# Performance work log

Hardware: AMD Instinct MI355X
Metric: run time of the kernel (lower is better)

Reference implementation:

```python
import jax, jax.numpy as jnp
import numpy as np

B, S, D, H = 4, 2048, 1024, 16
HD = D // H

def rotate_half(x):
    x1, x2 = jnp.split(x, 2, axis=-1)
    return jnp.concatenate((-x2, x1), axis=-1)

def apply_rope(x, cos, sin):
    # x: [B,H,S,hd]; cos/sin: [S,hd] -> broadcast over B,H
    return x * cos[None, None] + rotate_half(x) * sin[None, None]

def setup_inputs() -> dict:
    key = jax.random.key(0)
    ks = jax.random.split(key, 8)
    x = jax.random.normal(ks[0], (B, S, D), dtype=jnp.float32)
    mask = jnp.triu(jnp.ones((S, S), dtype=bool), k=1)  # True = masked (causal)
    pos = jnp.arange(S, dtype=jnp.float32)[:, None]
    inv = 1.0 / (10000.0 ** (jnp.arange(0, HD, 2, dtype=jnp.float32) / HD))
    ang = pos * inv[None, :]  # [S, hd/2]
    ang = jnp.concatenate([ang, ang], axis=-1)  # [S, hd]
    rope_cos = jnp.cos(ang)
    rope_sin = jnp.sin(ang)
    scale = 1.0 / np.sqrt(D)
    Wq = jax.random.normal(ks[1], (D, D), dtype=jnp.float32) * scale
    Wk = jax.random.normal(ks[2], (D, D), dtype=jnp.float32) * scale
    Wv = jax.random.normal(ks[3], (D, D), dtype=jnp.float32) * scale
    Wo = jax.random.normal(ks[4], (D, D), dtype=jnp.float32) * scale
    z = jnp.zeros((D,), dtype=jnp.float32)
    return {"x": x, "mask": mask, "rope_cos": rope_cos, "rope_sin": rope_sin,
            "Wq": Wq, "bq": z, "Wk": Wk, "bk": z, "Wv": Wv, "bv": z, "Wo": Wo, "bo": z}

def reference(x, mask, rope_cos, rope_sin, Wq, bq, Wk, bk, Wv, bv, Wo, bo):
    b, s, d = x.shape
    def proj(W, bias):
        y = x @ W.T + bias  # torch Linear: x W^T + b
        return y.reshape(b, s, H, HD).transpose(0, 2, 1, 3)  # [B,H,S,hd]
    Q = apply_rope(proj(Wq, bq), rope_cos, rope_sin)
    K = apply_rope(proj(Wk, bk), rope_cos, rope_sin)
    V = proj(Wv, bv)
    scores = jnp.einsum('bhqd,bhkd->bhqk', Q, K) / jnp.sqrt(jnp.float32(HD))
    scores = jnp.where(mask[None, None], -jnp.inf, scores)
    attn = jax.nn.softmax(scores, axis=-1)
    ctx = jnp.einsum('bhqk,bhkd->bhqd', attn, V)
    ctx = ctx.transpose(0, 2, 1, 3).reshape(b, s, d)
    return ctx @ Wo.T + bo
```

## Files before the change

kernel.cpp:

```cpp
#include <hip/hip_runtime.h>
#include <hip/hip_bf16.h>

#define S_LEN 2048
#define D_MODEL 1024
#define NH 16
#define HDIM 64
#define B_SZ 4

typedef __attribute__((ext_vector_type(8))) short bf16x8;
typedef __attribute__((ext_vector_type(4))) float f32x4;

__device__ inline void gld16(const __hip_bfloat16* g, __hip_bfloat16* l) {
    __builtin_amdgcn_global_load_lds(
        (const __attribute__((address_space(1))) unsigned int*)g,
        (__attribute__((address_space(3))) unsigned int*)l, 16, 0, 0);
}

__device__ inline unsigned int pkbf(float a, float b) {
    float2 f; f.x = a; f.y = b;
    __hip_bfloat162 h = __float22bfloat162_rn(f);
    union { __hip_bfloat162 h; unsigned int u; } cv; cv.h = h; return cv.u;
}

__global__ __launch_bounds__(256) void f2bf4_kernel(const float4* __restrict__ in,
                                                    __hip_bfloat162* __restrict__ out,
                                                    int n4) {
    int i = blockIdx.x * 256 + threadIdx.x;
    if (i < n4) {
        float4 v = in[i];
        __hip_bfloat162 a, b;
        a.x = __float2bfloat16(v.x); a.y = __float2bfloat16(v.y);
        b.x = __float2bfloat16(v.z); b.y = __float2bfloat16(v.w);
        out[2 * i]     = a;
        out[2 * i + 1] = b;
    }
}

__global__ __launch_bounds__(256) void f2bfw_kernel(
    const float4* __restrict__ w0, const float4* __restrict__ w1,
    const float4* __restrict__ w2, const float4* __restrict__ w3,
    __hip_bfloat162* __restrict__ o0, __hip_bfloat162* __restrict__ o1,
    __hip_bfloat162* __restrict__ o2, __hip_bfloat162* __restrict__ o3) {
    const int z = blockIdx.y;
    const float4* in = (z == 0) ? w0 : (z == 1) ? w1 : (z == 2) ? w2 : w3;
    __hip_bfloat162* out = (z == 0) ? o0 : (z == 1) ? o1 : (z == 2) ? o2 : o3;
    int i = blockIdx.x * 256 + threadIdx.x;
    float4 v = in[i];
    __hip_bfloat162 a, b;
    a.x = __float2bfloat16(v.x); a.y = __float2bfloat16(v.y);
    b.x = __float2bfloat16(v.z); b.y = __float2bfloat16(v.w);
    out[2 * i]     = a;
    out[2 * i + 1] = b;
}

__device__ inline void gemm_mainloop(const __hip_bfloat16* __restrict__ X,
                                     const __hip_bfloat16* __restrict__ W,
                                     __hip_bfloat16* As, __hip_bfloat16* Bs,
                                     int m0, int n0, f32x4 acc[4][4]) {
    const int tid = threadIdx.x;
    const int wv = tid >> 6, lane = tid & 63, l15 = lane & 15, quad = lane >> 4;
    const int rw = (wv >> 1) * 64, cw = (wv & 1) * 64;
    for (int k0 = 0; k0 < D_MODEL; k0 += 32) {
        __syncthreads();
#pragma unroll
        for (int i = 0; i < 2; i++) {
            int l = tid + 256 * i;
            int row = l >> 2, c8 = (l & 3) * 8;
            gld16(&X[(size_t)(m0 + row) * D_MODEL + k0 + c8], &As[row * 32 + c8]);
            gld16(&W[(size_t)(n0 + row) * D_MODEL + k0 + c8], &Bs[row * 32 + c8]);
        }
        __syncthreads();
        bf16x8 af[4], bfr[4];
#pragma unroll
        for (int t = 0; t < 4; t++)
            af[t] = *(const bf16x8*)&As[(rw + t * 16 + l15) * 32 + quad * 8];
#pragma unroll
        for (int t = 0; t < 4; t++)
            bfr[t] = *(const bf16x8*)&Bs[(cw + t * 16 + l15) * 32 + quad * 8];
#pragma unroll
        for (int mt = 0; mt < 4; mt++)
#pragma unroll
            for (int nt = 0; nt < 4; nt++)
                acc[mt][nt] = __builtin_amdgcn_mfma_f32_16x16x32_bf16(
                    af[mt], bfr[nt], acc[mt][nt], 0, 0, 0);
    }
}

#define PT 136
__global__ __launch_bounds__(256) void qkv_kernel(
    const __hip_bfloat16* __restrict__ X,
    const __hip_bfloat16* __restrict__ W0, const __hip_bfloat16* __restrict__ W1,
    const __hip_bfloat16* __restrict__ W2,
    const float* __restrict__ b0, const float* __restrict__ b1,
    const float* __restrict__ b2,
    const float* __restrict__ rc, const float* __restrict__ rs,
    __hip_bfloat16* __restrict__ Qo, __hip_bfloat16* __restrict__ Ko,
    __hip_bfloat16* __restrict__ Vo) {
    __shared__ __hip_bfloat16 pool[64 * PT];
    __hip_bfloat16* As = pool;
    __hip_bfloat16* Bs = pool + 4096;
    const int z = blockIdx.z;
    const __hip_bfloat16* W = (z == 0) ? W0 : ((z == 1) ? W1 : W2);
    const float* bias = (z == 0) ? b0 : ((z == 1) ? b1 : b2);
    f32x4 acc[4][4];
#pragma unroll
    for (int i = 0; i < 4; i++)
#pragma unroll
        for (int j = 0; j < 4; j++) acc[i][j] = (f32x4){0.f, 0.f, 0.f, 0.f};
    const int m0 = blockIdx.x * 128, n0 = blockIdx.y * 128;
    gemm_mainloop(X, W, As, Bs, m0, n0, acc);

    const int tid = threadIdx.x;
    const int wv = tid >> 6, lane = tid & 63, l15 = lane & 15, quad = lane >> 4;
    const int rw = (wv >> 1) * 64, cw = (wv & 1) * 64;

    if (z == 2) {
        __hip_bfloat16* T = pool;
        const int b = m0 >> 11, s0l = m0 & (S_LEN - 1);
#pragma unroll
        for (int hn = 0; hn < 2; hn++) {
            __syncthreads();
            if ((wv & 1) == hn) {
#pragma unroll
                for (int mt = 0; mt < 4; mt++)
#pragma unroll
                    for (int nt = 0; nt < 4; nt++)
#pragma unroll
                        for (int r = 0; r < 4; r++) {
                            int dl = nt * 16 + l15;
                            int ml = rw + mt * 16 + quad * 4 + r;
                            T[dl * PT + ml] =
                                __float2bfloat16(acc[mt][nt][r] + bias[n0 + hn * 64 + dl]);
                        }
            }
            __syncthreads();
            const int d = tid >> 2, sc = tid & 3;
            const int h = (n0 >> 6) + hn;
            size_t gb = ((size_t)((b * NH + h) * HDIM + d)) * S_LEN + s0l + sc * 32;
#pragma unroll
            for (int j = 0; j < 4; j++) {
                bf16x8 v = *(const bf16x8*)&T[d * PT + sc * 32 + j * 8];
                *(bf16x8*)&Vo[gb + j * 8] = v;
            }
        }
    } else {
        __hip_bfloat16* dst = (z == 0) ? Qo : Ko;
        const float qs = (z == 0) ? 0.18033688011112042f : 1.0f;
#pragma unroll
        for (int mt = 0; mt < 4; mt++)
#pragma unroll
            for (int r = 0; r < 4; r++) {
                int m = m0 + rw + mt * 16 + quad * 4 + r;
                int s = m & (S_LEN - 1), b = m >> 11;
#pragma unroll
                for (int nt = 0; nt < 2; nt++) {
                    int n1 = n0 + cw + nt * 16 + l15;
                    int h = n1 >> 6, hd1 = n1 & 63;
                    float y1 = acc[mt][nt][r] + bias[n1];
                    float y2 = acc[mt][nt + 2][r] + bias[n1 + 32];
                    float c1 = rc[s * HDIM + hd1], s1 = rs[s * HDIM + hd1];
                    float c2 = rc[s * HDIM + hd1 + 32], s2 = rs[s * HDIM + hd1 + 32];
                    size_t base = (((size_t)(b * NH + h)) * S_LEN + s) * HDIM;
                    dst[base + hd1]      = __float2bfloat16((y1 * c1 - y2 * s1) * qs);
                    dst[base + hd1 + 32] = __float2bfloat16((y2 * c2 + y1 * s2) * qs);
                }
            }
    }
}

#define SWZ(r, c) (((r) << 6) + ((c) ^ (((r) & 7) << 3)))
__global__ __launch_bounds__(256) void attn_kernel(
    const __hip_bfloat16* __restrict__ Q, const __hip_bfloat16* __restrict__ K,
    const __hip_bfloat16* __restrict__ VT, __hip_bfloat16* __restrict__ CTX) {
    __shared__ __hip_bfloat16 Kl[2][64 * 64];
    __shared__ __hip_bfloat16 Vl[2][64 * 64];
    __shared__ __hip_bfloat16 Pl[2][4][16 * 64];
    const int tid = threadIdx.x;
    const int wv = tid >> 6, lane = tid & 63, l15 = lane & 15, quad = lane >> 4;
    const int bh = blockIdx.x;
    const int pr = blockIdx.y;
    const int tA = pr, tC = 31 - pr;
    const int nkb = tC + 1;
    const size_t off = (size_t)bh * S_LEN * HDIM;
    const __hip_bfloat16* Qp = Q + off;
    const __hip_bfloat16* Kp = K + off;
    const __hip_bfloat16* Vp = VT + off;
    __hip_bfloat16* PC = &Pl[0][wv][0];
    __hip_bfloat16* PA = &Pl[1][wv][0];

    const int e0 = wv * 512 + lane * 8;
    const int r0 = e0 >> 6, c80 = e0 & 63;
    const int sw0 = c80 ^ ((r0 & 7) << 3);
    const int r1 = r0 + 32;
    const int sw1 = c80 ^ ((r1 & 7) << 3);
    const __hip_bfloat16* ks0 = Kp + r0 * 64 + sw0;
    const __hip_bfloat16* ks1 = Kp + r1 * 64 + sw1;
    const __hip_bfloat16* vs0 = Vp + (size_t)r0 * S_LEN + sw0;
    const __hip_bfloat16* vs1 = Vp + (size_t)r1 * S_LEN + sw1;

    auto stage = [&](int kb, int bsel) {
        const int ko = kb * 64;
        gld16(ks0 + (size_t)ko * 64, &Kl[bsel][e0]);
        gld16(ks1 + (size_t)ko * 64, &Kl[bsel][e0 + 2048]);
        gld16(vs0 + ko, &Vl[bsel][e0]);
        gld16(vs1 + ko, &Vl[bsel][e0 + 2048]);
    };

    bf16x8 qfA[2], qfC[2];
#pragma unroll
    for (int c = 0; c < 2; c++) {
        qfA[c] = *(const bf16x8*)&Qp[(size_t)(tA * 64 + wv * 16 + l15) * HDIM + c * 32 + quad * 8];
        qfC[c] = *(const bf16x8*)&Qp[(size_t)(tC * 64 + wv * 16 + l15) * HDIM + c * 32 + quad * 8];
    }

    float lA = 0.f, lC = 0.f;
    f32x4 accA[4], accC[4];
#pragma unroll
    for (int nt = 0; nt < 4; nt++) {
        accA[nt] = (f32x4){0.f, 0.f, 0.f, 0.f};
        accC[nt] = (f32x4){0.f, 0.f, 0.f, 0.f};
    }

    const int qrel = wv * 16 + l15;

    stage(0, 0);
    __syncthreads();
    for (int kb = 0; kb < nkb; kb++) {
        const int buf = kb & 1;
        if (kb + 1 < nkb) stage(kb + 1, buf ^ 1);
        const __hip_bfloat16* Kb_ = &Kl[buf][0];
        const __hip_bfloat16* Vb_ = &Vl[buf][0];

        const bool aAct = (kb <= tA);
        unsigned int pkC[8], pkA[8];

        f32x4 saC[4], saA[4];
#pragma unroll
        for (int st = 0; st < 4; st++) {
            saC[st] = (f32x4){0.f, 0.f, 0.f, 0.f};
            saA[st] = (f32x4){0.f, 0.f, 0.f, 0.f};
        }
        __builtin_amdgcn_s_setprio(1);
        if (aAct) {
#pragma unroll
            for (int c = 0; c < 2; c++)
#pragma unroll
                for (int st = 0; st < 4; st++) {
                    bf16x8 kf = *(const bf16x8*)&Kb_[SWZ(st * 16 + l15, c * 32 + quad * 8)];
                    saC[st] = __builtin_amdgcn_mfma_f32_16x16x32_bf16(kf, qfC[c], saC[st], 0, 0, 0);
                    saA[st] = __builtin_amdgcn_mfma_f32_16x16x32_bf16(kf, qfA[c], saA[st], 0, 0, 0);
                }
        } else {
#pragma unroll
            for (int c = 0; c < 2; c++)
#pragma unroll
                for (int st = 0; st < 4; st++) {
                    bf16x8 kf = *(const bf16x8*)&Kb_[SWZ(st * 16 + l15, c * 32 + quad * 8)];
                    saC[st] = __builtin_amdgcn_mfma_f32_16x16x32_bf16(kf, qfC[c], saC[st], 0, 0, 0);
                }
        }
        __builtin_amdgcn_s_setprio(0);

        {
            float ls = 0.f;
            if (kb == tC) {
#pragma unroll
                for (int st = 0; st < 4; st++) {
                    float p[4];
#pragma unroll
                    for (int r = 0; r < 4; r++) {
                        bool msk = (st * 16 + quad * 4 + r > qrel);
                        p[r] = msk ? 0.f : __builtin_exp2f(saC[st][r]);
                        ls += p[r];
                    }
                    pkC[st * 2 + 0] = pkbf(p[0], p[1]);
                    pkC[st * 2 + 1] = pkbf(p[2], p[3]);
                }
            } else {
#pragma unroll
                for (int st = 0; st < 4; st++) {
                    float p[4];
#pragma unroll
                    for (int r = 0; r < 4; r++) {
                        p[r] = __builtin_exp2f(saC[st][r]);
                        ls += p[r];
                    }
                    pkC[st * 2 + 0] = pkbf(p[0], p[1]);
                    pkC[st * 2 + 1] = pkbf(p[2], p[3]);
                }
            }
            ls += __shfl_xor(ls, 16);
            ls += __shfl_xor(ls, 32);
            lC += ls;
#pragma unroll
            for (int st = 0; st < 4; st++) {
                uint2 w; w.x = pkC[st * 2]; w.y = pkC[st * 2 + 1];
                *(uint2*)&PC[SWZ(l15, st * 16 + quad * 4)] = w;
            }
        }
        if (aAct) {
            float ls = 0.f;
            if (kb == tA) {
#pragma unroll
                for (int st = 0; st < 4; st++) {
                    float p[4];
#pragma unroll
                    for (int r = 0; r < 4; r++) {
                        bool msk = (st * 16 + quad * 4 + r > qrel);
                        p[r] = msk ? 0.f : __builtin_exp2f(saA[st][r]);
                        ls += p[r];
                    }
                    pkA[st * 2 + 0] = pkbf(p[0], p[1]);
                    pkA[st * 2 + 1] = pkbf(p[2], p[3]);
                }
            } else {
#pragma unroll
                for (int st = 0; st < 4; st++) {
                    float p[4];
#pragma unroll
                    for (int r = 0; r < 4; r++) {
                        p[r] = __builtin_exp2f(saA[st][r]);
                        ls += p[r];
                    }
                    pkA[st * 2 + 0] = pkbf(p[0], p[1]);
                    pkA[st * 2 + 1] = pkbf(p[2], p[3]);
                }
            }
            ls += __shfl_xor(ls, 16);
            ls += __shfl_xor(ls, 32);
            lA += ls;
#pragma unroll
            for (int st = 0; st < 4; st++) {
                uint2 w; w.x = pkA[st * 2]; w.y = pkA[st * 2 + 1];
                *(uint2*)&PA[SWZ(l15, st * 16 + quad * 4)] = w;
            }
        }

        __builtin_amdgcn_s_setprio(1);
#pragma unroll
        for (int c = 0; c < 2; c++) {
            bf16x8 vf[4];
#pragma unroll
            for (int nt = 0; nt < 4; nt++)
                vf[nt] = *(const bf16x8*)&Vb_[SWZ(nt * 16 + l15, c * 32 + quad * 8)];
            {
                bf16x8 pf = *(const bf16x8*)&PC[SWZ(l15, c * 32 + quad * 8)];
#pragma unroll
                for (int nt = 0; nt < 4; nt++)
                    accC[nt] = __builtin_amdgcn_mfma_f32_16x16x32_bf16(vf[nt], pf, accC[nt], 0, 0, 0);
            }
            if (aAct) {
                bf16x8 pf = *(const bf16x8*)&PA[SWZ(l15, c * 32 + quad * 8)];
#pragma unroll
                for (int nt = 0; nt < 4; nt++)
                    accA[nt] = __builtin_amdgcn_mfma_f32_16x16x32_bf16(vf[nt], pf, accA[nt], 0, 0, 0);
            }
        }
        __builtin_amdgcn_s_setprio(0);

        __syncthreads();
    }

    const int b = bh >> 4, h = bh & 15;
    {
        const int q = tA * 64 + wv * 16 + l15;
        const float inv = 1.0f / lA;
#pragma unroll
        for (int nt = 0; nt < 4; nt++) {
            uint2 st2;
            st2.x = pkbf(accA[nt][0] * inv, accA[nt][1] * inv);
            st2.y = pkbf(accA[nt][2] * inv, accA[nt][3] * inv);
            *(uint2*)&CTX[((size_t)(b * S_LEN + q)) * D_MODEL + h * HDIM + nt * 16 + quad * 4] = st2;
        }
    }
    {
        const int q = tC * 64 + wv * 16 + l15;
        const float inv = 1.0f / lC;
#pragma unroll
        for (int nt = 0; nt < 4; nt++) {
            uint2 st2;
            st2.x = pkbf(accC[nt][0] * inv, accC[nt][1] * inv);
            st2.y = pkbf(accC[nt][2] * inv, accC[nt][3] * inv);
            *(uint2*)&CTX[((size_t)(b * S_LEN + q)) * D_MODEL + h * HDIM + nt * 16 + quad * 4] = st2;
        }
    }
}

__global__ __launch_bounds__(256) void outproj_kernel(
    const __hip_bfloat16* __restrict__ X, const __hip_bfloat16* __restrict__ W,
    const float* __restrict__ bias, float* __restrict__ OUT) {
    __shared__ __hip_bfloat16 As[128 * 32];
    __shared__ __hip_bfloat16 Bs[128 * 32];
    f32x4 acc[4][4];
#pragma unroll
    for (int i = 0; i < 4; i++)
#pragma unroll
        for (int j = 0; j < 4; j++) acc[i][j] = (f32x4){0.f, 0.f, 0.f, 0.f};
    const int m0 = blockIdx.x * 128, n0 = blockIdx.y * 128;
    gemm_mainloop(X, W, As, Bs, m0, n0, acc);
    const int tid = threadIdx.x;
    const int wv = tid >> 6, lane = tid & 63, l15 = lane & 15, quad = lane >> 4;
    const int rw = (wv >> 1) * 64, cw = (wv & 1) * 64;
#pragma unroll
    for (int mt = 0; mt < 4; mt++)
#pragma unroll
        for (int r = 0; r < 4; r++) {
            int m = m0 + rw + mt * 16 + quad * 4 + r;
#pragma unroll
            for (int nt = 0; nt < 4; nt++) {
                int n = n0 + cw + nt * 16 + l15;
                OUT[(size_t)m * D_MODEL + n] = acc[mt][nt][r] + bias[n];
            }
        }
}

extern "C" void kernel_launch(void* const* d_in, const int* in_sizes, int n_in,
                              void* d_out, int out_size, void* d_ws, size_t ws_size,
                              hipStream_t stream) {
    const float* x  = (const float*)d_in[0];
    const float* rc = (const float*)d_in[2];
    const float* rs = (const float*)d_in[3];
    const float* Wq = (const float*)d_in[4];
    const float* bq = (const float*)d_in[5];
    const float* Wk = (const float*)d_in[6];
    const float* bk = (const float*)d_in[7];
    const float* Wv = (const float*)d_in[8];
    const float* bv = (const float*)d_in[9];
    const float* Wo = (const float*)d_in[10];
    const float* bo = (const float*)d_in[11];

    char* ws = (char*)d_ws;
    __hip_bfloat16* xbf = (__hip_bfloat16*)(ws);
    __hip_bfloat16* wqb = (__hip_bfloat16*)(ws + (16u << 20));
    __hip_bfloat16* wkb = (__hip_bfloat16*)(ws + (18u << 20));
    __hip_bfloat16* wvb = (__hip_bfloat16*)(ws + (20u << 20));
    __hip_bfloat16* wob = (__hip_bfloat16*)(ws + (22u << 20));
    __hip_bfloat16* Qb  = (__hip_bfloat16*)(ws + (24u << 20));
    __hip_bfloat16* Kb  = (__hip_bfloat16*)(ws + (40u << 20));
    __hip_bfloat16* Vb  = (__hip_bfloat16*)(ws + (56u << 20));
    __hip_bfloat16* Cb  = (__hip_bfloat16*)(ws + (72u << 20));
    float* out = (float*)d_out;

    f2bf4_kernel<<<8192, 256, 0, stream>>>((const float4*)x, (__hip_bfloat162*)xbf, 2097152);
    f2bfw_kernel<<<dim3(1024, 4), 256, 0, stream>>>(
        (const float4*)Wq, (const float4*)Wk, (const float4*)Wv, (const float4*)Wo,
        (__hip_bfloat162*)wqb, (__hip_bfloat162*)wkb, (__hip_bfloat162*)wvb,
        (__hip_bfloat162*)wob);

    qkv_kernel<<<dim3(64, 8, 3), 256, 0, stream>>>(xbf, wqb, wkb, wvb, bq, bk, bv,
                                                   rc, rs, Qb, Kb, Vb);
    attn_kernel<<<dim3(64, 16), 256, 0, stream>>>(Qb, Kb, Vb, Cb);
    outproj_kernel<<<dim3(64, 8), 256, 0, stream>>>(Cb, wob, bo, out);
}
```

Measured before the change: 313.0 us.

## Replace GEMM mainloop with 256x256 double-buffered ping-pong MFMA pipeline

The QKV and output-projection GEMMs now use 512-thread blocks computing 256x256 tiles with a K-step of 64. Tiles sit in XOR-swizzled, double-buffered LDS (128KB of dynamic shared memory) and are loaded with async global-to-LDS copies interleaved between four MFMA phases per step, using barriers and setprio. The aim is to raise arithmetic intensity and overlap global loads with matrix math. Separately, the setprio calls are removed from the attention kernel. The trade-off is far fewer blocks: 384 for QKV and only 128 for the output projection, with one block per CU given the LDS use, so the output projection may leave many CUs idle.

Result: slower. 320.9 us (+2.5%).

```diff
diff --git a/kernel.cpp b/kernel.cpp
--- a/kernel.cpp
+++ b/kernel.cpp
@@ -53,41 +53,133 @@
     out[2 * i + 1] = b;
 }
 
-__device__ inline void gemm_mainloop(const __hip_bfloat16* __restrict__ X,
-                                     const __hip_bfloat16* __restrict__ W,
-                                     __hip_bfloat16* As, __hip_bfloat16* Bs,
-                                     int m0, int n0, f32x4 acc[4][4]) {
+__device__ inline void gemm8p(const __hip_bfloat16* __restrict__ X,
+                              const __hip_bfloat16* __restrict__ W,
+                              __hip_bfloat16* Al, __hip_bfloat16* Bl,
+                              int m0, int n0, f32x4 acc[4][8]) {
     const int tid = threadIdx.x;
     const int wv = tid >> 6, lane = tid & 63, l15 = lane & 15, quad = lane >> 4;
-    const int rw = (wv >> 1) * 64, cw = (wv & 1) * 64;
-    for (int k0 = 0; k0 < D_MODEL; k0 += 32) {
-        __syncthreads();
-#pragma unroll
-        for (int i = 0; i < 2; i++) {
-            int l = tid + 256 * i;
-            int row = l >> 2, c8 = (l & 3) * 8;
-            gld16(&X[(size_t)(m0 + row) * D_MODEL + k0 + c8], &As[row * 32 + c8]);
-            gld16(&W[(size_t)(n0 + row) * D_MODEL + k0 + c8], &Bs[row * 32 + c8]);
-        }
-        __syncthreads();
-        bf16x8 af[4], bfr[4];
-#pragma unroll
-        for (int t = 0; t < 4; t++)
-            af[t] = *(const bf16x8*)&As[(rw + t * 16 + l15) * 32 + quad * 8];
-#pragma unroll
-        for (int t = 0; t < 4; t++)
-            bfr[t] = *(const bf16x8*)&Bs[(cw + t * 16 + l15) * 32 + quad * 8];
-#pragma unroll
-        for (int mt = 0; mt < 4; mt++)
-#pragma unroll
-            for (int nt = 0; nt < 4; nt++)
-                acc[mt][nt] = __builtin_amdgcn_mfma_f32_16x16x32_bf16(
-                    af[mt], bfr[nt], acc[mt][nt], 0, 0, 0);
-    }
-}
-
-#define PT 136
-__global__ __launch_bounds__(256) void qkv_kernel(
+    const int wr = wv >> 1, wc = wv & 1;
+    const int l7 = l15 & 7;
+    const int wr16l = wr * 16 + l15;
+    const int wc16l = wc * 16 + l15;
+    const int sr = tid >> 3;
+    const int sc8 = ((tid & 7) ^ (sr & 7)) * 8;
+    const __hip_bfloat16* xs = X + (size_t)(m0 + sr) * D_MODEL + sc8;
+    const __hip_bfloat16* ws = W + (size_t)(n0 + sr) * D_MODEL + sc8;
+    const int ldd = tid * 8;
+
+#define SA8(bf_, h_, kt_) { \
+    gld16(xs + (size_t)((h_)*128)      * D_MODEL + (kt_)*64, Al + (bf_)*16384 + ((h_)*2)*4096 + ldd); \
+    gld16(xs + (size_t)((h_)*128 + 64) * D_MODEL + (kt_)*64, Al + (bf_)*16384 + ((h_)*2+1)*4096 + ldd); }
+#define SB8(bf_, h_, kt_) { \
+    gld16(ws + (size_t)((h_)*128)      * D_MODEL + (kt_)*64, Bl + (bf_)*16384 + ((h_)*2)*4096 + ldd); \
+    gld16(ws + (size_t)((h_)*128 + 64) * D_MODEL + (kt_)*64, Bl + (bf_)*16384 + ((h_)*2+1)*4096 + ldd); }
+
+    SB8(0, 0, 0); SA8(0, 0, 0); SB8(0, 1, 0); SA8(0, 1, 0);
+    SB8(1, 0, 1); SA8(1, 0, 1); SB8(1, 1, 1);
+    asm volatile("s_waitcnt vmcnt(6)" ::: "memory");
+    __builtin_amdgcn_s_barrier();
+
+    for (int t = 0; t < 16; t++) {
+        const int buf = t & 1;
+        const __hip_bfloat16* Ab = Al + buf * 16384;
+        const __hip_bfloat16* Bb = Bl + buf * 16384;
+        bf16x8 af[2][2], bfr[4][2];
+
+#pragma unroll
+        for (int nl = 0; nl < 4; nl++)
+#pragma unroll
+            for (int kc = 0; kc < 2; kc++)
+                bfr[nl][kc] = *(const bf16x8*)&Bb[(nl * 32 + wc16l) * 64 + ((kc * 4 + quad) ^ l7) * 8];
+#pragma unroll
+        for (int ml = 0; ml < 2; ml++)
+#pragma unroll
+            for (int kc = 0; kc < 2; kc++)
+                af[ml][kc] = *(const bf16x8*)&Ab[(ml * 64 + wr16l) * 64 + ((kc * 4 + quad) ^ l7) * 8];
+        if (t + 1 < 16) SA8(buf ^ 1, 1, t + 1);
+        __builtin_amdgcn_s_barrier();
+        __builtin_amdgcn_s_setprio(1);
+#pragma unroll
+        for (int ml = 0; ml < 2; ml++)
+#pragma unroll
+            for (int nl = 0; nl < 4; nl++)
+#pragma unroll
+                for (int kc = 0; kc < 2; kc++)
+                    acc[ml][nl] = __builtin_amdgcn_mfma_f32_16x16x32_bf16(
+                        af[ml][kc], bfr[nl][kc], acc[ml][nl], 0, 0, 0);
+        __builtin_amdgcn_s_setprio(0);
+        __builtin_amdgcn_s_barrier();
+
+#pragma unroll
+        for (int ml = 0; ml < 2; ml++)
+#pragma unroll
+            for (int kc = 0; kc < 2; kc++)
+                af[ml][kc] = *(const bf16x8*)&Ab[(128 + ml * 64 + wr16l) * 64 + ((kc * 4 + quad) ^ l7) * 8];
+        if (t + 2 < 16) SB8(buf, 0, t + 2);
+        __builtin_amdgcn_s_barrier();
+        __builtin_amdgcn_s_setprio(1);
+#pragma unroll
+        for (int ml = 0; ml < 2; ml++)
+#pragma unroll
+            for (int nl = 0; nl < 4; nl++)
+#pragma unroll
+                for (int kc = 0; kc < 2; kc++)
+                    acc[2 + ml][nl] = __builtin_amdgcn_mfma_f32_16x16x32_bf16(
+                        af[ml][kc], bfr[nl][kc], acc[2 + ml][nl], 0, 0, 0);
+        __builtin_amdgcn_s_setprio(0);
+        __builtin_amdgcn_s_barrier();
+
+#pragma unroll
+        for (int nl = 0; nl < 4; nl++)
+#pragma unroll
+            for (int kc = 0; kc < 2; kc++)
+                bfr[nl][kc] = *(const bf16x8*)&Bb[(128 + nl * 32 + wc16l) * 64 + ((kc * 4 + quad) ^ l7) * 8];
+#pragma unroll
+        for (int ml = 0; ml < 2; ml++)
+#pragma unroll
+            for (int kc = 0; kc < 2; kc++)
+                af[ml][kc] = *(const bf16x8*)&Ab[(ml * 64 + wr16l) * 64 + ((kc * 4 + quad) ^ l7) * 8];
+        __builtin_amdgcn_s_barrier();
+        __builtin_amdgcn_s_setprio(1);
+#pragma unroll
+        for (int ml = 0; ml < 2; ml++)
+#pragma unroll
+            for (int nl = 0; nl < 4; nl++)
+#pragma unroll
+                for (int kc = 0; kc < 2; kc++)
+                    acc[ml][4 + nl] = __builtin_amdgcn_mfma_f32_16x16x32_bf16(
+                        af[ml][kc], bfr[nl][kc], acc[ml][4 + nl], 0, 0, 0);
+        __builtin_amdgcn_s_setprio(0);
+        __builtin_amdgcn_s_barrier();
+
+#pragma unroll
+        for (int ml = 0; ml < 2; ml++)
+#pragma unroll
+            for (int kc = 0; kc < 2; kc++)
+                af[ml][kc] = *(const bf16x8*)&Ab[(128 + ml * 64 + wr16l) * 64 + ((kc * 4 + quad) ^ l7) * 8];
+        if (t + 2 < 16) { SA8(buf, 0, t + 2); SB8(buf, 1, t + 2); }
+        __builtin_amdgcn_s_barrier();
+        __builtin_amdgcn_s_setprio(1);
+#pragma unroll
+        for (int ml = 0; ml < 2; ml++)
+#pragma unroll
+            for (int nl = 0; nl < 4; nl++)
+#pragma unroll
+                for (int kc = 0; kc < 2; kc++)
+                    acc[2 + ml][4 + nl] = __builtin_amdgcn_mfma_f32_16x16x32_bf16(
+                        af[ml][kc], bfr[nl][kc], acc[2 + ml][4 + nl], 0, 0, 0);
+        __builtin_amdgcn_s_setprio(0);
+        if (t == 14)      asm volatile("s_waitcnt vmcnt(0)" ::: "memory");
+        else if (t < 14)  asm volatile("s_waitcnt vmcnt(6)" ::: "memory");
+        __builtin_amdgcn_s_barrier();
+    }
+#undef SA8
+#undef SB8
+}
+
+#define PT8 264
+__global__ __launch_bounds__(512, 2) void qkv_kernel(
     const __hip_bfloat16* __restrict__ X,
     const __hip_bfloat16* __restrict__ W0, const __hip_bfloat16* __restrict__ W1,
     const __hip_bfloat16* __restrict__ W2,
@@ -96,76 +188,76 @@
     const float* __restrict__ rc, const float* __restrict__ rs,
     __hip_bfloat16* __restrict__ Qo, __hip_bfloat16* __restrict__ Ko,
     __hip_bfloat16* __restrict__ Vo) {
-    __shared__ __hip_bfloat16 pool[64 * PT];
-    __hip_bfloat16* As = pool;
-    __hip_bfloat16* Bs = pool + 4096;
+    extern __shared__ __hip_bfloat16 lds[];
+    __hip_bfloat16* Al = lds;
+    __hip_bfloat16* Bl = lds + 32768;
     const int z = blockIdx.z;
     const __hip_bfloat16* W = (z == 0) ? W0 : ((z == 1) ? W1 : W2);
     const float* bias = (z == 0) ? b0 : ((z == 1) ? b1 : b2);
-    f32x4 acc[4][4];
+    f32x4 acc[4][8];
 #pragma unroll
     for (int i = 0; i < 4; i++)
 #pragma unroll
-        for (int j = 0; j < 4; j++) acc[i][j] = (f32x4){0.f, 0.f, 0.f, 0.f};
-    const int m0 = blockIdx.x * 128, n0 = blockIdx.y * 128;
-    gemm_mainloop(X, W, As, Bs, m0, n0, acc);
+        for (int j = 0; j < 8; j++) acc[i][j] = (f32x4){0.f, 0.f, 0.f, 0.f};
+    const int m0 = blockIdx.x * 256, n0 = blockIdx.y * 256;
+    gemm8p(X, W, Al, Bl, m0, n0, acc);
 
     const int tid = threadIdx.x;
     const int wv = tid >> 6, lane = tid & 63, l15 = lane & 15, quad = lane >> 4;
-    const int rw = (wv >> 1) * 64, cw = (wv & 1) * 64;
+    const int wr = wv >> 1, wc = wv & 1;
 
     if (z == 2) {
-        __hip_bfloat16* T = pool;
+        __hip_bfloat16* T = Al;
         const int b = m0 >> 11, s0l = m0 & (S_LEN - 1);
 #pragma unroll
-        for (int hn = 0; hn < 2; hn++) {
+        for (int j = 0; j < 4; j++) {
             __syncthreads();
-            if ((wv & 1) == hn) {
-#pragma unroll
-                for (int mt = 0; mt < 4; mt++)
-#pragma unroll
-                    for (int nt = 0; nt < 4; nt++)
-#pragma unroll
-                        for (int r = 0; r < 4; r++) {
-                            int dl = nt * 16 + l15;
-                            int ml = rw + mt * 16 + quad * 4 + r;
-                            T[dl * PT + ml] =
-                                __float2bfloat16(acc[mt][nt][r] + bias[n0 + hn * 64 + dl]);
-                        }
-            }
+#pragma unroll
+            for (int mt = 0; mt < 4; mt++)
+#pragma unroll
+                for (int e = 0; e < 2; e++) {
+                    int hd = e * 32 + wc * 16 + l15;
+#pragma unroll
+                    for (int r = 0; r < 4; r++) {
+                        int mloc = mt * 64 + wr * 16 + quad * 4 + r;
+                        T[hd * PT8 + mloc] =
+                            __float2bfloat16(acc[mt][2 * j + e][r] + bias[n0 + j * 64 + hd]);
+                    }
+                }
             __syncthreads();
-            const int d = tid >> 2, sc = tid & 3;
-            const int h = (n0 >> 6) + hn;
+            const int d = tid >> 3, sc = tid & 7;
+            const int h = (n0 >> 6) + j;
             size_t gb = ((size_t)((b * NH + h) * HDIM + d)) * S_LEN + s0l + sc * 32;
 #pragma unroll
+            for (int j8 = 0; j8 < 4; j8++) {
+                bf16x8 v = *(const bf16x8*)&T[d * PT8 + sc * 32 + j8 * 8];
+                *(bf16x8*)&Vo[gb + j8 * 8] = v;
+            }
+        }
+        return;
+    }
+
+    __hip_bfloat16* dst = (z == 0) ? Qo : Ko;
+    const float qs = (z == 0) ? 0.18033688011112042f : 1.0f;
+    const int hd1 = wc * 16 + l15;
+#pragma unroll
+    for (int mt = 0; mt < 4; mt++)
+#pragma unroll
+        for (int r = 0; r < 4; r++) {
+            int m = m0 + mt * 64 + wr * 16 + quad * 4 + r;
+            int s = m & (S_LEN - 1), b = m >> 11;
+            float c1 = rc[s * HDIM + hd1], s1 = rs[s * HDIM + hd1];
+            float c2 = rc[s * HDIM + hd1 + 32], s2 = rs[s * HDIM + hd1 + 32];
+#pragma unroll
             for (int j = 0; j < 4; j++) {
-                bf16x8 v = *(const bf16x8*)&T[d * PT + sc * 32 + j * 8];
-                *(bf16x8*)&Vo[gb + j * 8] = v;
-            }
-        }
-    } else {
-        __hip_bfloat16* dst = (z == 0) ? Qo : Ko;
-        const float qs = (z == 0) ? 0.18033688011112042f : 1.0f;
-#pragma unroll
-        for (int mt = 0; mt < 4; mt++)
-#pragma unroll
-            for (int r = 0; r < 4; r++) {
-                int m = m0 + rw + mt * 16 + quad * 4 + r;
-                int s = m & (S_LEN - 1), b = m >> 11;
-#pragma unroll
-                for (int nt = 0; nt < 2; nt++) {
-                    int n1 = n0 + cw + nt * 16 + l15;
-                    int h = n1 >> 6, hd1 = n1 & 63;
-                    float y1 = acc[mt][nt][r] + bias[n1];
-                    float y2 = acc[mt][nt + 2][r] + bias[n1 + 32];
-                    float c1 = rc[s * HDIM + hd1], s1 = rs[s * HDIM + hd1];
-                    float c2 = rc[s * HDIM + hd1 + 32], s2 = rs[s * HDIM + hd1 + 32];
-                    size_t base = (((size_t)(b * NH + h)) * S_LEN + s) * HDIM;
-                    dst[base + hd1]      = __float2bfloat16((y1 * c1 - y2 * s1) * qs);
-                    dst[base + hd1 + 32] = __float2bfloat16((y2 * c2 + y1 * s2) * qs);
-                }
-            }
-    }
+                int h = (n0 >> 6) + j;
+                float y1 = acc[mt][2 * j][r] + bias[n0 + j * 64 + hd1];
+                float y2 = acc[mt][2 * j + 1][r] + bias[n0 + j * 64 + hd1 + 32];
+                size_t base = (((size_t)(b * NH + h)) * S_LEN + s) * HDIM;
+                dst[base + hd1]      = __float2bfloat16((y1 * c1 - y2 * s1) * qs);
+                dst[base + hd1 + 32] = __float2bfloat16((y2 * c2 + y1 * s2) * qs);
+            }
+        }
 }
 
 #define SWZ(r, c) (((r) << 6) + ((c) ^ (((r) & 7) << 3)))
@@ -240,7 +332,6 @@
             saC[st] = (f32x4){0.f, 0.f, 0.f, 0.f};
             saA[st] = (f32x4){0.f, 0.f, 0.f, 0.f};
         }
-        __builtin_amdgcn_s_setprio(1);
         if (aAct) {
 #pragma unroll
             for (int c = 0; c < 2; c++)
@@ -259,7 +350,6 @@
                     saC[st] = __builtin_amdgcn_mfma_f32_16x16x32_bf16(kf, qfC[c], saC[st], 0, 0, 0);
                 }
         }
-        __builtin_amdgcn_s_setprio(0);
 
         {
             float ls = 0.f;
@@ -336,7 +426,6 @@
             }
         }
 
-        __builtin_amdgcn_s_setprio(1);
 #pragma unroll
         for (int c = 0; c < 2; c++) {
             bf16x8 vf[4];
@@ -356,7 +445,6 @@
                     accA[nt] = __builtin_amdgcn_mfma_f32_16x16x32_bf16(vf[nt], pf, accA[nt], 0, 0, 0);
             }
         }
-        __builtin_amdgcn_s_setprio(0);
 
         __syncthreads();
     }
@@ -386,29 +474,30 @@
     }
 }
 
-__global__ __launch_bounds__(256) void outproj_kernel(
+__global__ __launch_bounds__(512, 2) void outproj_kernel(
     const __hip_bfloat16* __restrict__ X, const __hip_bfloat16* __restrict__ W,
     const float* __restrict__ bias, float* __restrict__ OUT) {
-    __shared__ __hip_bfloat16 As[128 * 32];
-    __shared__ __hip_bfloat16 Bs[128 * 32];
-    f32x4 acc[4][4];
+    extern __shared__ __hip_bfloat16 lds[];
+    __hip_bfloat16* Al = lds;
+    __hip_bfloat16* Bl = lds + 32768;
+    f32x4 acc[4][8];
 #pragma unroll
     for (int i = 0; i < 4; i++)
 #pragma unroll
-        for (int j = 0; j < 4; j++) acc[i][j] = (f32x4){0.f, 0.f, 0.f, 0.f};
-    const int m0 = blockIdx.x * 128, n0 = blockIdx.y * 128;
-    gemm_mainloop(X, W, As, Bs, m0, n0, acc);
+        for (int j = 0; j < 8; j++) acc[i][j] = (f32x4){0.f, 0.f, 0.f, 0.f};
+    const int m0 = blockIdx.x * 256, n0 = blockIdx.y * 256;
+    gemm8p(X, W, Al, Bl, m0, n0, acc);
     const int tid = threadIdx.x;
     const int wv = tid >> 6, lane = tid & 63, l15 = lane & 15, quad = lane >> 4;
-    const int rw = (wv >> 1) * 64, cw = (wv & 1) * 64;
+    const int wr = wv >> 1, wc = wv & 1;
 #pragma unroll
     for (int mt = 0; mt < 4; mt++)
 #pragma unroll
         for (int r = 0; r < 4; r++) {
-            int m = m0 + rw + mt * 16 + quad * 4 + r;
-#pragma unroll
-            for (int nt = 0; nt < 4; nt++) {
-                int n = n0 + cw + nt * 16 + l15;
+            int m = m0 + mt * 64 + wr * 16 + quad * 4 + r;
+#pragma unroll
+            for (int nt = 0; nt < 8; nt++) {
+                int n = n0 + nt * 32 + wc * 16 + l15;
                 OUT[(size_t)m * D_MODEL + n] = acc[mt][nt][r] + bias[n];
             }
         }
@@ -441,14 +530,19 @@
     __hip_bfloat16* Cb  = (__hip_bfloat16*)(ws + (72u << 20));
     float* out = (float*)d_out;
 
+    (void)hipFuncSetAttribute((const void*)qkv_kernel,
+                              hipFuncAttributeMaxDynamicSharedMemorySize, 131072);
+    (void)hipFuncSetAttribute((const void*)outproj_kernel,
+                              hipFuncAttributeMaxDynamicSharedMemorySize, 131072);
+
     f2bf4_kernel<<<8192, 256, 0, stream>>>((const float4*)x, (__hip_bfloat162*)xbf, 2097152);
     f2bfw_kernel<<<dim3(1024, 4), 256, 0, stream>>>(
         (const float4*)Wq, (const float4*)Wk, (const float4*)Wv, (const float4*)Wo,
         (__hip_bfloat162*)wqb, (__hip_bfloat162*)wkb, (__hip_bfloat162*)wvb,
         (__hip_bfloat162*)wob);
 
-    qkv_kernel<<<dim3(64, 8, 3), 256, 0, stream>>>(xbf, wqb, wkb, wvb, bq, bk, bv,
-                                                   rc, rs, Qb, Kb, Vb);
+    qkv_kernel<<<dim3(32, 4, 3), 512, 131072, stream>>>(xbf, wqb, wkb, wvb, bq, bk, bv,
+                                                        rc, rs, Qb, Kb, Vb);
     attn_kernel<<<dim3(64, 16), 256, 0, stream>>>(Qb, Kb, Vb, Cb);
-    outproj_kernel<<<dim3(64, 8), 256, 0, stream>>>(Cb, wob, bo, out);
-}
+    outproj_kernel<<<dim3(32, 4), 512, 131072, stream>>>(Cb, wob, bo, out);
+}
```
